# Kernel optimization log

Hardware: AMD Instinct MI355X
Metric: run time of the kernel (lower is better)

## Reference

```python
import jax, jax.numpy as jnp
import numpy as np

N_NODES = 50000
N_EDGES = 800000
D_IN = 128
D_HID = 256


def setup_inputs() -> dict:
    key = jax.random.key(0)
    ks = jax.random.split(key, 8)
    x = jax.random.normal(ks[0], (N_NODES, D_IN), dtype=jnp.float32)
    edge_index = jax.random.randint(ks[1], (2, N_EDGES), 0, N_NODES, dtype=jnp.int32)
    s1 = 1.0 / np.sqrt(D_IN)
    s2 = 1.0 / np.sqrt(D_HID)
    W1_l = jax.random.uniform(ks[2], (D_IN, D_HID), jnp.float32, -s1, s1)
    W1_r = jax.random.uniform(ks[3], (D_IN, D_HID), jnp.float32, -s1, s1)
    b1 = jax.random.uniform(ks[4], (D_HID,), jnp.float32, -s1, s1)
    W2_l = jax.random.uniform(ks[5], (D_HID, D_HID), jnp.float32, -s2, s2)
    W2_r = jax.random.uniform(ks[6], (D_HID, D_HID), jnp.float32, -s2, s2)
    b2 = jax.random.uniform(ks[7], (D_HID,), jnp.float32, -s2, s2)
    return {"x": x, "edge_index": edge_index,
            "W1_l": W1_l, "W1_r": W1_r, "b1": b1,
            "W2_l": W2_l, "W2_r": W2_r, "b2": b2}


def _sage_conv(x, src, dst, deg_inv, W_l, W_r, b):
    # mean-aggregate neighbor features at destination nodes, then
    # out = lin_l(mean_neighbors) + lin_r(x)  (PyG SAGEConv, mean aggr)
    msgs = x[src]                                              # [E, d]  irregular gather
    agg = jax.ops.segment_sum(msgs, dst, num_segments=x.shape[0])  # [N, d] scatter-add
    mean = agg * deg_inv[:, None]
    return mean @ W_l + x @ W_r + b


def reference(x, edge_index, W1_l, W1_r, b1, W2_l, W2_r, b2):
    src, dst = edge_index[0], edge_index[1]
    n = x.shape[0]
    deg = jax.ops.segment_sum(jnp.ones_like(dst, dtype=x.dtype), dst, num_segments=n)
    deg_inv = jnp.where(deg > 0, 1.0 / jnp.maximum(deg, 1.0), 0.0)
    h = jax.nn.relu(_sage_conv(x, src, dst, deg_inv, W1_l, W1_r, b1))
    # dropout is identity in eval mode
    out = jax.nn.relu(_sage_conv(h, src, dst, deg_inv, W2_l, W2_r, b2))
    return out
```

## Files before the change

kernel.cpp:

```cpp
#include <hip/hip_runtime.h>
#include <hip/hip_bf16.h>


#define DIN 128
#define DH  256
#define ELLW 64
#define NCONV 512

typedef __attribute__((ext_vector_type(8))) short short8v;
typedef __attribute__((ext_vector_type(4))) float float4v;
typedef __attribute__((ext_vector_type(2))) float float2v;

__device__ __forceinline__ void gload_lds16(const void* g, void* l) {
    __builtin_amdgcn_global_load_lds((const __attribute__((address_space(1))) void*)g,
                                     (__attribute__((address_space(3))) void*)l, 16, 0, 0);
}
__device__ __forceinline__ float bf2f(unsigned short u) {
    union { unsigned int i; float f; } c; c.i = ((unsigned int)u) << 16; return c.f;
}
__device__ __forceinline__ unsigned short f2bf(float f) {
    union { float f; unsigned int i; } c; c.f = f;
    unsigned int lsb = (c.i >> 16) & 1u;
    return (unsigned short)((c.i + 0x7fffu + lsb) >> 16);
}
__device__ __host__ __forceinline__ int permcol(int q) {
    return ((q >> 6) << 6) + ((q & 3) << 4) + ((q >> 2) & 15);
}
__device__ __host__ __forceinline__ int permout(int p) {
    return (((p >> 6) << 4) + (p & 15)) * 4 + ((p >> 4) & 3);
}

__global__ __launch_bounds__(256) void prologue(const float* __restrict__ x,
                                                const float* __restrict__ W1l,
                                                const float* __restrict__ W1r,
                                                const float* __restrict__ W2l,
                                                const float* __restrict__ W2r,
                                                unsigned short* __restrict__ Wt1,
                                                unsigned short* __restrict__ Wt2,
                                                unsigned short* __restrict__ Acat1,
                                                unsigned char* __restrict__ xf8,
                                                const int* __restrict__ src,
                                                const int* __restrict__ dst,
                                                int* __restrict__ cnt,
                                                unsigned short* __restrict__ ell,
                                                int N, int E) {
    const int tid = threadIdx.x;

    if (blockIdx.x < NCONV) {
        const int gtid = blockIdx.x * 256 + tid;
        const int nthr = NCONV * 256;

        for (int id = gtid; id < 256 * 256 + 256 * 512; id += nthr) {
            if (id < 256 * 256) {
                int n = id >> 8, k = id & 255;
                float v = (k < 128) ? W1l[k * 256 + n] : W1r[(k - 128) * 256 + n];
                Wt1[n * 256 + k] = f2bf(v);
            } else {
                int id2 = id - 256 * 256;
                int n = id2 >> 9, k = id2 & 511;
                int tc = permout(n);
                float v = (k < 256) ? W2l[permcol(k) * 256 + tc]
                                    : W2r[permcol(k - 256) * 256 + tc];
                Wt2[n * 512 + k] = f2bf(v);
            }
        }
        for (int id = gtid; id < N * 32; id += nthr) {
            int base = id * 4;
            float4 v = *(const float4*)(x + base);
            int row = base >> 7, c = base & 127;
            ushort4 o;
            o.x = f2bf(v.x); o.y = f2bf(v.y); o.z = f2bf(v.z); o.w = f2bf(v.w);
            *(ushort4*)(Acat1 + (size_t)row * 256 + 128 + c) = o;
            int p = __builtin_amdgcn_cvt_pk_fp8_f32(v.x, v.y, 0, false);
            p = __builtin_amdgcn_cvt_pk_fp8_f32(v.z, v.w, p, true);
            *(unsigned int*)(xf8 + (size_t)row * 128 + c) = (unsigned int)p;
        }
    } else {
        int idx = blockIdx.x - NCONV;
        int xc = idx & 7;
        int bslot = idx >> 3;
        int nslot = (gridDim.x - NCONV) >> 3;
        int per = (((E + nslot - 1) / nslot) + 7) & ~7;
        int lo = bslot * per;
        int hi = min(lo + per, E);
        for (int base = lo + tid * 8; base + 7 < hi; base += 256 * 8) {
            int4 da = *(const int4*)(dst + base);
            int4 db = *(const int4*)(dst + base + 4);
            int4 sa = *(const int4*)(src + base);
            int4 sb = *(const int4*)(src + base + 4);
            int dd[8] = {da.x, da.y, da.z, da.w, db.x, db.y, db.z, db.w};
            int ss[8] = {sa.x, sa.y, sa.z, sa.w, sb.x, sb.y, sb.z, sb.w};
#pragma unroll
            for (int q = 0; q < 8; ++q) {
                if (((dd[q] >> 6) & 7) == xc) {
                    int p = atomicAdd(&cnt[dd[q]], 1);
                    if (p < ELLW) ell[(size_t)dd[q] * ELLW + p] = (unsigned short)ss[q];
                }
            }
        }
        int tail = lo + ((hi > lo ? (hi - lo) : 0) & ~7);
        if (tid < (hi - tail)) {
            int e = tail + tid;
            int d = dst[e];
            if (((d >> 6) & 7) == xc) {
                int p = atomicAdd(&cnt[d], 1);
                if (p < ELLW) ell[(size_t)d * ELLW + p] = (unsigned short)src[e];
            }
        }
    }
}

template <int ROWB, int WSTR>
__global__ __launch_bounds__(256) void agg_wpn(const unsigned char* __restrict__ f8,
                                               const unsigned short* __restrict__ ell,
                                               const int* __restrict__ cnt,
                                               unsigned short* __restrict__ outp, int N) {
    constexpr int LANES = ROWB / 4;
    constexpr int NPB = 256 / LANES;
    int tid = threadIdx.x;
    int node = blockIdx.x * NPB + tid / LANES;
    int lane = tid % LANES;
    if (node >= N) return;
    int cn = cnt[node];
    int dg = min(cn, ELLW);
    const unsigned short* row = ell + (size_t)node * ELLW;
    const unsigned char* fb = f8 + (size_t)lane * 4;
    float a0 = 0.f, a1 = 0.f, a2 = 0.f, a3 = 0.f;
    int j = 0;
    for (; j + 16 <= dg; j += 16) {
        short8v i8a = *(const short8v*)(row + j);
        short8v i8b = *(const short8v*)(row + j + 8);
        unsigned int v[16];
#pragma unroll
        for (int q = 0; q < 8; ++q)
            v[q] = *(const unsigned int*)(fb + (size_t)(unsigned short)i8a[q] * ROWB);
#pragma unroll
        for (int q = 0; q < 8; ++q)
            v[8 + q] = *(const unsigned int*)(fb + (size_t)(unsigned short)i8b[q] * ROWB);
#pragma unroll
        for (int q = 0; q < 16; ++q) {
            float2v lo = __builtin_amdgcn_cvt_pk_f32_fp8((int)v[q], false);
            float2v hi = __builtin_amdgcn_cvt_pk_f32_fp8((int)v[q], true);
            a0 += lo[0]; a1 += lo[1]; a2 += hi[0]; a3 += hi[1];
        }
    }
    for (; j + 8 <= dg; j += 8) {
        short8v i8 = *(const short8v*)(row + j);
        unsigned int v[8];
#pragma unroll
        for (int q = 0; q < 8; ++q)
            v[q] = *(const unsigned int*)(fb + (size_t)(unsigned short)i8[q] * ROWB);
#pragma unroll
        for (int q = 0; q < 8; ++q) {
            float2v lo = __builtin_amdgcn_cvt_pk_f32_fp8((int)v[q], false);
            float2v hi = __builtin_amdgcn_cvt_pk_f32_fp8((int)v[q], true);
            a0 += lo[0]; a1 += lo[1]; a2 += hi[0]; a3 += hi[1];
        }
    }
    for (; j < dg; ++j) {
        unsigned int v = *(const unsigned int*)(fb + (size_t)row[j] * ROWB);
        float2v lo = __builtin_amdgcn_cvt_pk_f32_fp8((int)v, false);
        float2v hi = __builtin_amdgcn_cvt_pk_f32_fp8((int)v, true);
        a0 += lo[0]; a1 += lo[1]; a2 += hi[0]; a3 += hi[1];
    }
    float di = (cn > 0) ? 1.0f / (float)cn : 0.0f;
    ushort4 o;
    o.x = f2bf(a0 * di); o.y = f2bf(a1 * di);
    o.z = f2bf(a2 * di); o.w = f2bf(a3 * di);
    *(ushort4*)(outp + (size_t)node * WSTR + lane * 4) = o;
}

template <int OUT_BF16>
__global__ __launch_bounds__(512) void gemm_mfma(const unsigned short* __restrict__ A, int lda,
                                                 const unsigned short* __restrict__ Wt, int K,
                                                 const float* __restrict__ bias,
                                                 float* __restrict__ outF,
                                                 unsigned short* __restrict__ outB, int ldo,
                                                 unsigned char* __restrict__ outF8,
                                                 int M) {
    __shared__ __align__(16) char lds[49152];
    char* ldsA = lds;
    char* ldsB = lds + 16384;

    const int tid = threadIdx.x;
    const int lane = tid & 63;
    const int wid = tid >> 6;
    const int wm = wid >> 2, wn = wid & 3;
    const int m0 = blockIdx.x * 128;

    float4v acc[4][4];
#pragma unroll
    for (int i = 0; i < 4; ++i)
#pragma unroll
        for (int j = 0; j < 4; ++j) acc[i][j] = (float4v)(0.f);

    int rA[2], cA[2], rB[4], cB[4];
#pragma unroll
    for (int i = 0; i < 2; ++i) {
        int blin = i * 8192 + tid * 16;
        int bdat = blin ^ (((blin >> 7) & 7) << 4);
        rA[i] = min(m0 + (bdat >> 7), M - 1);
        cA[i] = (bdat & 127) >> 1;
    }
#pragma unroll
    for (int i = 0; i < 4; ++i) {
        int blin = i * 8192 + tid * 16;
        int bdat = blin ^ (((blin >> 7) & 7) << 4);
        rB[i] = bdat >> 7;
        cB[i] = (bdat & 127) >> 1;
    }

    for (int kc = 0; kc < K; kc += 64) {
#pragma unroll
        for (int i = 0; i < 2; ++i)
            gload_lds16(A + (size_t)rA[i] * lda + kc + cA[i],
                        ldsA + i * 8192 + wid * 1024);
#pragma unroll
        for (int i = 0; i < 4; ++i)
            gload_lds16(Wt + (size_t)rB[i] * K + kc + cB[i],
                        ldsB + i * 8192 + wid * 1024);
        __syncthreads();

#pragma unroll
        for (int ks = 0; ks < 2; ++ks) {
            short8v af[4], bf[4];
            int cbyte = (ks * 32 + ((lane >> 4) << 3)) * 2;
#pragma unroll
            for (int mi = 0; mi < 4; ++mi) {
                int r = wm * 64 + mi * 16 + (lane & 15);
                int bdat = (r << 7) + cbyte;
                int blin = bdat ^ (((r & 7)) << 4);
                af[mi] = *(const short8v*)(ldsA + blin);
            }
#pragma unroll
            for (int ni = 0; ni < 4; ++ni) {
                int r = wn * 64 + ni * 16 + (lane & 15);
                int bdat = (r << 7) + cbyte;
                int blin = bdat ^ (((r & 7)) << 4);
                bf[ni] = *(const short8v*)(ldsB + blin);
            }
#pragma unroll
            for (int mi = 0; mi < 4; ++mi)
#pragma unroll
                for (int ni = 0; ni < 4; ++ni)
                    acc[mi][ni] = __builtin_amdgcn_mfma_f32_16x16x32_bf16(
                        af[mi], bf[ni], acc[mi][ni], 0, 0, 0);
        }
        __syncthreads();
    }

    const int cl = lane & 15;
    const int rq = (lane >> 4) * 4;
    if (OUT_BF16) {
        const int pbase = (wn * 16 + cl) * 4;
        float bvn[4];
#pragma unroll
        for (int ni = 0; ni < 4; ++ni) bvn[ni] = bias[wn * 64 + ni * 16 + cl];
#pragma unroll
        for (int mi = 0; mi < 4; ++mi) {
#pragma unroll
            for (int j = 0; j < 4; ++j) {
                int gr = m0 + wm * 64 + mi * 16 + rq + j;
                if (gr < M) {
                    float v0 = fmaxf(acc[mi][0][j] + bvn[0], 0.f);
                    float v1 = fmaxf(acc[mi][1][j] + bvn[1], 0.f);
                    float v2 = fmaxf(acc[mi][2][j] + bvn[2], 0.f);
                    float v3 = fmaxf(acc[mi][3][j] + bvn[3], 0.f);
                    ushort4 hb;
                    hb.x = f2bf(v0); hb.y = f2bf(v1);
                    hb.z = f2bf(v2); hb.w = f2bf(v3);
                    *(ushort4*)(outB + (size_t)gr * ldo + pbase) = hb;
                    int pb = __builtin_amdgcn_cvt_pk_fp8_f32(v0, v1, 0, false);
                    pb = __builtin_amdgcn_cvt_pk_fp8_f32(v2, v3, pb, true);
                    *(unsigned int*)(outF8 + (size_t)gr * 256 + pbase) = (unsigned int)pb;
                }
            }
        }
    } else {
        const int obase = (wn * 16 + cl) * 4;
        float4 bv = *(const float4*)(bias + obase);
#pragma unroll
        for (int mi = 0; mi < 4; ++mi) {
#pragma unroll
            for (int j = 0; j < 4; ++j) {
                int gr = m0 + wm * 64 + mi * 16 + rq + j;
                if (gr < M) {
                    float4 o;
                    o.x = fmaxf(acc[mi][0][j] + bv.x, 0.f);
                    o.y = fmaxf(acc[mi][1][j] + bv.y, 0.f);
                    o.z = fmaxf(acc[mi][2][j] + bv.z, 0.f);
                    o.w = fmaxf(acc[mi][3][j] + bv.w, 0.f);
                    *(float4*)(outF + (size_t)gr * 256 + obase) = o;
                }
            }
        }
    }
}

extern "C" void kernel_launch(void* const* d_in, const int* in_sizes, int n_in,
                              void* d_out, int out_size, void* d_ws, size_t ws_size,
                              hipStream_t stream) {
    const float* x   = (const float*)d_in[0];
    const int*   ei  = (const int*)d_in[1];
    const float* W1l = (const float*)d_in[2];
    const float* W1r = (const float*)d_in[3];
    const float* b1  = (const float*)d_in[4];
    const float* W2l = (const float*)d_in[5];
    const float* W2r = (const float*)d_in[6];
    const float* b2  = (const float*)d_in[7];
    float* out = (float*)d_out;

    int N = in_sizes[0] / DIN;
    int E = in_sizes[1] / 2;
    const int* srcI = ei;
    const int* dstI = ei + E;

    char* w = (char*)d_ws;
    auto alloc = [&](size_t bytes) -> char* {
        char* p = w;
        w += (bytes + 255) & ~(size_t)255;
        return p;
    };
    int* cnt = (int*)alloc((size_t)N * 4);
    unsigned short* ell = (unsigned short*)alloc((size_t)N * ELLW * 2);
    unsigned short* Acat1 = (unsigned short*)alloc((size_t)N * 256 * 2);
    unsigned short* Acat2 = (unsigned short*)alloc((size_t)N * 512 * 2);
    unsigned short* Wt1   = (unsigned short*)alloc((size_t)256 * 256 * 2);
    unsigned short* Wt2   = (unsigned short*)alloc((size_t)256 * 512 * 2);
    unsigned char*  hf8   = (unsigned char*)alloc((size_t)N * 256);
    unsigned char*  xf8   = (unsigned char*)Acat2;

    (void)hipMemsetAsync(cnt, 0, (size_t)N * 4, stream);
    prologue<<<2048, 256, 0, stream>>>(x, W1l, W1r, W2l, W2r, Wt1, Wt2,
                                       Acat1, xf8, srcI, dstI, cnt, ell, N, E);

    int gridM = (N + 127) / 128;

    agg_wpn<128, 256><<<(N + 7) / 8, 256, 0, stream>>>(xf8, ell, cnt, Acat1, N);
    gemm_mfma<1><<<gridM, 512, 0, stream>>>(Acat1, 256, Wt1, 256, b1,
                                            nullptr, Acat2 + 256, 512, hf8, N);
    agg_wpn<256, 512><<<(N + 3) / 4, 256, 0, stream>>>(hf8, ell, cnt, Acat2, N);
    gemm_mfma<0><<<gridM, 512, 0, stream>>>(Acat2, 512, Wt2, 512, b2,
                                            out, nullptr, 256, nullptr, N);
}
```

Baseline: 151.5 us.

## Fuse neighbor aggregation into GEMM kernel per 128-row tile

Merges the separate aggregation kernel into the GEMM kernel. Each 512-thread block first gathers and mean-aggregates the 128 nodes of its own tile, writes them to the A buffer, syncs, then runs the MFMA GEMM. This removes two kernel launches and lets the GEMM read freshly written rows that are likely still in cache. In exchange, the gather phase now runs at lower occupancy (512-thread blocks that reserve 48KB LDS) with no overlap between gather and GEMM inside a block. xf8 gets its own buffer because layer-1's fused kernel writes into Acat2 while xf8 may still be read.

```diff
diff --git a/kernel.cpp b/kernel.cpp
--- a/kernel.cpp
+++ b/kernel.cpp
@@ -49,7 +49,6 @@
     if (blockIdx.x < NCONV) {
         const int gtid = blockIdx.x * 256 + tid;
         const int nthr = NCONV * 256;
-
         for (int id = gtid; id < 256 * 256 + 256 * 512; id += nthr) {
             if (id < 256 * 256) {
                 int n = id >> 8, k = id & 255;
@@ -110,83 +109,88 @@
     }
 }
 
-template <int ROWB, int WSTR>
-__global__ __launch_bounds__(256) void agg_wpn(const unsigned char* __restrict__ f8,
-                                               const unsigned short* __restrict__ ell,
-                                               const int* __restrict__ cnt,
-                                               unsigned short* __restrict__ outp, int N) {
-    constexpr int LANES = ROWB / 4;
-    constexpr int NPB = 256 / LANES;
-    int tid = threadIdx.x;
-    int node = blockIdx.x * NPB + tid / LANES;
-    int lane = tid % LANES;
-    if (node >= N) return;
-    int cn = cnt[node];
-    int dg = min(cn, ELLW);
-    const unsigned short* row = ell + (size_t)node * ELLW;
-    const unsigned char* fb = f8 + (size_t)lane * 4;
-    float a0 = 0.f, a1 = 0.f, a2 = 0.f, a3 = 0.f;
-    int j = 0;
-    for (; j + 16 <= dg; j += 16) {
-        short8v i8a = *(const short8v*)(row + j);
-        short8v i8b = *(const short8v*)(row + j + 8);
-        unsigned int v[16];
-#pragma unroll
-        for (int q = 0; q < 8; ++q)
-            v[q] = *(const unsigned int*)(fb + (size_t)(unsigned short)i8a[q] * ROWB);
-#pragma unroll
-        for (int q = 0; q < 8; ++q)
-            v[8 + q] = *(const unsigned int*)(fb + (size_t)(unsigned short)i8b[q] * ROWB);
-#pragma unroll
-        for (int q = 0; q < 16; ++q) {
-            float2v lo = __builtin_amdgcn_cvt_pk_f32_fp8((int)v[q], false);
-            float2v hi = __builtin_amdgcn_cvt_pk_f32_fp8((int)v[q], true);
-            a0 += lo[0]; a1 += lo[1]; a2 += hi[0]; a3 += hi[1];
-        }
-    }
-    for (; j + 8 <= dg; j += 8) {
-        short8v i8 = *(const short8v*)(row + j);
-        unsigned int v[8];
-#pragma unroll
-        for (int q = 0; q < 8; ++q)
-            v[q] = *(const unsigned int*)(fb + (size_t)(unsigned short)i8[q] * ROWB);
-#pragma unroll
-        for (int q = 0; q < 8; ++q) {
-            float2v lo = __builtin_amdgcn_cvt_pk_f32_fp8((int)v[q], false);
-            float2v hi = __builtin_amdgcn_cvt_pk_f32_fp8((int)v[q], true);
-            a0 += lo[0]; a1 += lo[1]; a2 += hi[0]; a3 += hi[1];
-        }
-    }
-    for (; j < dg; ++j) {
-        unsigned int v = *(const unsigned int*)(fb + (size_t)row[j] * ROWB);
-        float2v lo = __builtin_amdgcn_cvt_pk_f32_fp8((int)v, false);
-        float2v hi = __builtin_amdgcn_cvt_pk_f32_fp8((int)v, true);
-        a0 += lo[0]; a1 += lo[1]; a2 += hi[0]; a3 += hi[1];
-    }
-    float di = (cn > 0) ? 1.0f / (float)cn : 0.0f;
-    ushort4 o;
-    o.x = f2bf(a0 * di); o.y = f2bf(a1 * di);
-    o.z = f2bf(a2 * di); o.w = f2bf(a3 * di);
-    *(ushort4*)(outp + (size_t)node * WSTR + lane * 4) = o;
-}
-
-template <int OUT_BF16>
-__global__ __launch_bounds__(512) void gemm_mfma(const unsigned short* __restrict__ A, int lda,
-                                                 const unsigned short* __restrict__ Wt, int K,
-                                                 const float* __restrict__ bias,
-                                                 float* __restrict__ outF,
-                                                 unsigned short* __restrict__ outB, int ldo,
-                                                 unsigned char* __restrict__ outF8,
-                                                 int M) {
+template <int OUT_BF16, int ROWB>
+__global__ __launch_bounds__(512) void agg_gemm(const unsigned char* __restrict__ f8,
+                                                const unsigned short* __restrict__ ell,
+                                                const int* __restrict__ cnt,
+                                                unsigned short* __restrict__ A, int lda,
+                                                const unsigned short* __restrict__ Wt, int K,
+                                                const float* __restrict__ bias,
+                                                float* __restrict__ outF,
+                                                unsigned short* __restrict__ outB, int ldo,
+                                                unsigned char* __restrict__ outF8,
+                                                int M) {
     __shared__ __align__(16) char lds[49152];
     char* ldsA = lds;
     char* ldsB = lds + 16384;
 
     const int tid = threadIdx.x;
+    const int m0 = blockIdx.x * 128;
+
+    {
+        constexpr int LANES = ROWB / 4;
+        constexpr int NPB = 512 / LANES;
+        const int lane = tid % LANES;
+        const int nsub = tid / LANES;
+        const unsigned char* fb = f8 + (size_t)lane * 4;
+#pragma unroll 1
+        for (int p = 0; p < 128 / NPB; ++p) {
+            int node = m0 + p * NPB + nsub;
+            if (node < M) {
+                int cn = cnt[node];
+                int dg = min(cn, ELLW);
+                const unsigned short* row = ell + (size_t)node * ELLW;
+                float a0 = 0.f, a1 = 0.f, a2 = 0.f, a3 = 0.f;
+                int j = 0;
+                for (; j + 16 <= dg; j += 16) {
+                    short8v i8a = *(const short8v*)(row + j);
+                    short8v i8b = *(const short8v*)(row + j + 8);
+                    unsigned int v[16];
+#pragma unroll
+                    for (int q = 0; q < 8; ++q)
+                        v[q] = *(const unsigned int*)(fb + (size_t)(unsigned short)i8a[q] * ROWB);
+#pragma unroll
+                    for (int q = 0; q < 8; ++q)
+                        v[8 + q] = *(const unsigned int*)(fb + (size_t)(unsigned short)i8b[q] * ROWB);
+#pragma unroll
+                    for (int q = 0; q < 16; ++q) {
+                        float2v lo = __builtin_amdgcn_cvt_pk_f32_fp8((int)v[q], false);
+                        float2v hi = __builtin_amdgcn_cvt_pk_f32_fp8((int)v[q], true);
+                        a0 += lo[0]; a1 += lo[1]; a2 += hi[0]; a3 += hi[1];
+                    }
+                }
+                for (; j + 8 <= dg; j += 8) {
+                    short8v i8 = *(const short8v*)(row + j);
+                    unsigned int v[8];
+#pragma unroll
+                    for (int q = 0; q < 8; ++q)
+                        v[q] = *(const unsigned int*)(fb + (size_t)(unsigned short)i8[q] * ROWB);
+#pragma unroll
+                    for (int q = 0; q < 8; ++q) {
+                        float2v lo = __builtin_amdgcn_cvt_pk_f32_fp8((int)v[q], false);
+                        float2v hi = __builtin_amdgcn_cvt_pk_f32_fp8((int)v[q], true);
+                        a0 += lo[0]; a1 += lo[1]; a2 += hi[0]; a3 += hi[1];
+                    }
+                }
+                for (; j < dg; ++j) {
+                    unsigned int v = *(const unsigned int*)(fb + (size_t)row[j] * ROWB);
+                    float2v lo = __builtin_amdgcn_cvt_pk_f32_fp8((int)v, false);
+                    float2v hi = __builtin_amdgcn_cvt_pk_f32_fp8((int)v, true);
+                    a0 += lo[0]; a1 += lo[1]; a2 += hi[0]; a3 += hi[1];
+                }
+                float di = (cn > 0) ? 1.0f / (float)cn : 0.0f;
+                ushort4 o;
+                o.x = f2bf(a0 * di); o.y = f2bf(a1 * di);
+                o.z = f2bf(a2 * di); o.w = f2bf(a3 * di);
+                *(ushort4*)(A + (size_t)node * lda + lane * 4) = o;
+            }
+        }
+    }
+    __syncthreads();
+
     const int lane = tid & 63;
     const int wid = tid >> 6;
     const int wm = wid >> 2, wn = wid & 3;
-    const int m0 = blockIdx.x * 128;
 
     float4v acc[4][4];
 #pragma unroll
@@ -328,7 +332,7 @@
     unsigned short* Wt1   = (unsigned short*)alloc((size_t)256 * 256 * 2);
     unsigned short* Wt2   = (unsigned short*)alloc((size_t)256 * 512 * 2);
     unsigned char*  hf8   = (unsigned char*)alloc((size_t)N * 256);
-    unsigned char*  xf8   = (unsigned char*)Acat2;
+    unsigned char*  xf8   = (unsigned char*)alloc((size_t)N * 128);
 
     (void)hipMemsetAsync(cnt, 0, (size_t)N * 4, stream);
     prologue<<<2048, 256, 0, stream>>>(x, W1l, W1r, W2l, W2r, Wt1, Wt2,
@@ -336,10 +340,10 @@
 
     int gridM = (N + 127) / 128;
 
-    agg_wpn<128, 256><<<(N + 7) / 8, 256, 0, stream>>>(xf8, ell, cnt, Acat1, N);
-    gemm_mfma<1><<<gridM, 512, 0, stream>>>(Acat1, 256, Wt1, 256, b1,
-                                            nullptr, Acat2 + 256, 512, hf8, N);
-    agg_wpn<256, 512><<<(N + 3) / 4, 256, 0, stream>>>(hf8, ell, cnt, Acat2, N);
-    gemm_mfma<0><<<gridM, 512, 0, stream>>>(Acat2, 512, Wt2, 512, b2,
-                                            out, nullptr, 256, nullptr, N);
-}
+    agg_gemm<1, 128><<<gridM, 512, 0, stream>>>(xf8, ell, cnt, Acat1, 256,
+                                                Wt1, 256, b1,
+                                                nullptr, Acat2 + 256, 512, hf8, N);
+    agg_gemm<0, 256><<<gridM, 512, 0, stream>>>(hf8, ell, cnt, Acat2, 512,
+                                                Wt2, 512, b2,
+                                                out, nullptr, 256, nullptr, N);
+}
```

Measured after the change: 191.7 us. +26.6%, slower.
